# Optimization experiments

Hardware: AMD Instinct MI355X
Metric: run time of the kernel (lower is better)

Reference implementation:

```python
import jax, jax.numpy as jnp
import numpy as np

D_MODEL = 1024
N_HEADS = 16
N_KV = 4
HEAD_DIM = D_MODEL // N_HEADS
B, T, CACHE_LEN = 2, 1024, 1024
MAX_SEQ = 4096
ROPE_BASE = 10000.0


def _rope_tables(max_seq_len=MAX_SEQ, head_dim=HEAD_DIM, base=ROPE_BASE):
    inv_freq = 1.0 / (base ** (np.arange(0, head_dim, 2, dtype=np.float32) / head_dim))
    t = np.arange(max_seq_len, dtype=np.float32)
    freqs = np.outer(t, inv_freq)                      # [S, hd/2]
    emb = np.concatenate([freqs, freqs], axis=-1)      # [S, hd]
    return jnp.asarray(np.cos(emb)), jnp.asarray(np.sin(emb))


def _rotate_half(x):
    x1, x2 = jnp.split(x, 2, axis=-1)
    return jnp.concatenate([-x2, x1], axis=-1)


def setup_inputs() -> dict:
    key = jax.random.key(0)
    ks = jax.random.split(key, 8)
    return {
        "x": jax.random.normal(ks[0], (B, T, D_MODEL), dtype=jnp.float32),
        "k_cache": jax.random.normal(ks[1], (B, N_KV, CACHE_LEN, HEAD_DIM), dtype=jnp.float32),
        "v_cache": jax.random.normal(ks[2], (B, N_KV, CACHE_LEN, HEAD_DIM), dtype=jnp.float32),
        "position_indices": jax.random.randint(ks[3], (B, T), 0, 1024, dtype=jnp.int32),
        "Wq": jax.random.normal(ks[4], (D_MODEL, D_MODEL), dtype=jnp.float32) * 0.02,
        "Wk": jax.random.normal(ks[5], (D_MODEL, N_KV * HEAD_DIM), dtype=jnp.float32) * 0.02,
        "Wv": jax.random.normal(ks[6], (D_MODEL, N_KV * HEAD_DIM), dtype=jnp.float32) * 0.02,
        "Wo": jax.random.normal(ks[7], (D_MODEL, D_MODEL), dtype=jnp.float32) * 0.02,
    }


def reference(x, k_cache, v_cache, position_indices, Wq, Wk, Wv, Wo):
    Bq, Tq, C = x.shape
    n_kv, cache_len, hd = k_cache.shape[1], k_cache.shape[2], k_cache.shape[3]
    n_heads = Wq.shape[1] // hd
    n_rep = n_heads // n_kv
    scale = hd ** -0.5

    cos, sin = _rope_tables()

    # projections -> [B, H, T, hd]
    q = (x @ Wq).reshape(Bq, Tq, n_heads, hd).transpose(0, 2, 1, 3)
    k = (x @ Wk).reshape(Bq, Tq, n_kv, hd).transpose(0, 2, 1, 3)
    v = (x @ Wv).reshape(Bq, Tq, n_kv, hd).transpose(0, 2, 1, 3)

    # progress-aware RoPE: position-indexed gather into tables, offset by cache len
    offset = cache_len
    t_seq = jnp.arange(Tq, dtype=jnp.int32)[None, :] + offset          # [1, T]
    idx = jnp.clip(position_indices.astype(jnp.int32) + t_seq, 0, cos.shape[0] - 1)  # [B, T]
    cos_b = cos[idx][:, None]  # [B, 1, T, hd]
    sin_b = sin[idx][:, None]
    q = q * cos_b + _rotate_half(q) * sin_b
    k = k * cos_b + _rotate_half(k) * sin_b

    # KV-cache concat
    k = jnp.concatenate([k_cache, k], axis=2)  # [B, n_kv, S, hd]
    v = jnp.concatenate([v_cache, v], axis=2)

    # GQA head expansion (repeat each kv head n_rep times, contiguous grouping)
    k_exp = jnp.repeat(k, n_rep, axis=1)  # [B, H, S, hd]
    v_exp = jnp.repeat(v, n_rep, axis=1)

    # manual attention path (k_cache provided -> NO causal mask, matching torch code)
    attn = jnp.einsum("bhtd,bhsd->bhts", q, k_exp) * scale
    attn = jax.nn.softmax(attn, axis=-1)
    out = jnp.einsum("bhts,bhsd->bhtd", attn, v_exp)
    out = out.transpose(0, 2, 1, 3).reshape(Bq, Tq, C)
    return out @ Wo, k, v
```

## Files before the change

kernel.cpp:

```cpp
#include <hip/hip_runtime.h>
#include <hip/hip_bf16.h>
#include <stdint.h>

#define D_MODEL 1024
#define N_HEADS 16
#define N_KV 4
#define HD 64
#define BB 2
#define TT 1024
#define CACHE_LEN 1024
#define SS 2048
#define MAX_SEQ 4096
#define QKV_N 1536
#define NROWS 32768
#define GRP_EL (SS * HD)
#define NSP 4

typedef __attribute__((ext_vector_type(8))) short bf16x8;
typedef __attribute__((ext_vector_type(4))) float f32x4;

__device__ inline short f2bs(float f) {
    __hip_bfloat16 h = __float2bfloat16(f);
    return *reinterpret_cast<short*>(&h);
}
__device__ inline float bs2f(short s) {
    return __uint_as_float((unsigned)(unsigned short)s << 16);
}

__device__ inline int kfrag_off(int s, int d) {
    return (s >> 4) * 1024 + ((d >= 32) ? 512 : 0) + ((((d & 31) >> 3) * 16 + (s & 15)) * 8) + (d & 7);
}
__device__ inline int vfrag_off(int s, int d) {
    return ((s >> 5) * 4 + (d >> 4)) * 512 + ((((s >> 2) & 3) * 16 + (d & 15)) * 8)
         + (((s >> 4) & 1) * 4) + (s & 3);
}

__device__ void transp_body(const float* __restrict__ src, short* __restrict__ dst,
                            int N, int bx, int by) {
    __shared__ short tile[32][34];
    int tx = threadIdx.x & 31, ty = threadIdx.x >> 5;
    int n0 = bx * 32, k0 = by * 32;
#pragma unroll
    for (int i = 0; i < 4; i++)
        tile[ty + i * 8][tx] = f2bs(src[(size_t)(k0 + ty + i * 8) * N + n0 + tx]);
    __syncthreads();
#pragma unroll
    for (int i = 0; i < 4; i++)
        dst[(size_t)(n0 + ty + i * 8) * 1024 + k0 + tx] = tile[tx][ty + i * 8];
}

__global__ void k_prep(const float* __restrict__ x, short* __restrict__ xb,
                       const float* __restrict__ Wq, const float* __restrict__ Wk,
                       const float* __restrict__ Wv, const float* __restrict__ Wo,
                       short* __restrict__ Wt, short* __restrict__ Wot) {
    int id = blockIdx.x;
    if (id < 2048) {
        int i = (id * 256 + threadIdx.x) * 4;
        float4 v = *reinterpret_cast<const float4*>(x + i);
        short4 o = make_short4(f2bs(v.x), f2bs(v.y), f2bs(v.z), f2bs(v.w));
        *reinterpret_cast<short4*>(xb + i) = o;
        return;
    }
    id -= 2048;
    if (id < 1024) { transp_body(Wq, Wt, 1024, id & 31, id >> 5); return; }
    id -= 1024;
    if (id < 256)  { transp_body(Wk, Wt + (size_t)1024 * 1024, 256, id & 7, id >> 3); return; }
    id -= 256;
    if (id < 256)  { transp_body(Wv, Wt + (size_t)1280 * 1024, 256, id & 7, id >> 3); return; }
    id -= 256;
    transp_body(Wo, Wot, 1024, id & 31, id >> 5);
}

template <bool BF16_OUT>
__global__ __launch_bounds__(256) void k_gemm_bt(
    const short* __restrict__ A, const short* __restrict__ Bt, void* __restrict__ Cv,
    int M, int N, int K) {
    __shared__ short sA[64 * 32];
    __shared__ short sB[128 * 32];
    int m0 = blockIdx.y * 64, n0 = blockIdx.x * 128;
    int g = threadIdx.x;
    int lane = g & 63, wave = g >> 6;
    int wr = wave >> 1, wc = wave & 1;
    int quad = lane >> 4, l15 = lane & 15;

    f32x4 acc[2][4] = {};

    for (int k0 = 0; k0 < K; k0 += 32) {
        __syncthreads();
        {
            int row = g >> 2, col = (g & 3) << 3;
            const short* gpA = A + (size_t)(m0 + row) * K + k0 + col;
            __builtin_amdgcn_global_load_lds(
                (const __attribute__((address_space(1))) void*)gpA,
                (__attribute__((address_space(3))) void*)((char*)sA + wave * 1024), 16, 0, 0);
        }
#pragma unroll
        for (int it = 0; it < 2; it++) {
            int c = it * 256 + g;
            int row = c >> 2, col = (c & 3) << 3;
            const short* gpB = Bt + (size_t)(n0 + row) * K + k0 + col;
            __builtin_amdgcn_global_load_lds(
                (const __attribute__((address_space(1))) void*)gpB,
                (__attribute__((address_space(3))) void*)((char*)sB + (it * 256 + wave * 64) * 16), 16, 0, 0);
        }
        __syncthreads();
        bf16x8 af[2], bfr[4];
#pragma unroll
        for (int i = 0; i < 2; i++)
            af[i] = *reinterpret_cast<const bf16x8*>(sA + (wr * 32 + i * 16 + l15) * 32 + quad * 8);
#pragma unroll
        for (int j = 0; j < 4; j++)
            bfr[j] = *reinterpret_cast<const bf16x8*>(sB + (wc * 64 + j * 16 + l15) * 32 + quad * 8);
#pragma unroll
        for (int i = 0; i < 2; i++)
#pragma unroll
            for (int j = 0; j < 4; j++)
                acc[i][j] = __builtin_amdgcn_mfma_f32_16x16x32_bf16(af[i], bfr[j], acc[i][j], 0, 0, 0);
    }
#pragma unroll
    for (int i = 0; i < 2; i++) {
        int m = m0 + wr * 32 + i * 16 + quad * 4;
#pragma unroll
        for (int j = 0; j < 4; j++) {
            int n = n0 + wc * 64 + j * 16 + l15;
#pragma unroll
            for (int r = 0; r < 4; r++) {
                if constexpr (BF16_OUT)
                    ((short*)Cv)[(size_t)(m + r) * N + n] = f2bs(acc[i][j][r]);
                else
                    ((float*)Cv)[(size_t)(m + r) * N + n] = acc[i][j][r];
            }
        }
    }
}

__global__ void k_rope(const short* __restrict__ qkvb, const int* __restrict__ pos,
                       short* __restrict__ qb, short* __restrict__ kf,
                       float* __restrict__ k_out) {
    int row = blockIdx.x;
    int b = row >> 10, t = row & 1023;
    int g = threadIdx.x;
    __shared__ float scv[32], ssv[32];
    if (g < 32) {
        int idx = pos[row] + t + CACHE_LEN;
        idx = min(max(idx, 0), MAX_SEQ - 1);
        float inv = expf(-(float)g * (9.210340371976184f / 32.0f));
        sincosf((float)idx * inv, &ssv[g], &scv[g]);
    }
    __syncthreads();
    const short* src = qkvb + (size_t)row * QKV_N;
    const float QS = 0.18033688011112042f;

#pragma unroll
    for (int p = g; p < 512; p += 256) {
        int h = p >> 5, i = p & 31;
        float cv = scv[i], sv = ssv[i];
        float x1 = bs2f(src[h * 64 + i]), x2 = bs2f(src[h * 64 + i + 32]);
        size_t qbase = ((size_t)(b * N_HEADS + h) * TT + t) * HD;
        qb[qbase + i]      = f2bs((x1 * cv - x2 * sv) * QS);
        qb[qbase + i + 32] = f2bs((x2 * cv + x1 * sv) * QS);
    }
    if (g < 128) {
        int h = g >> 5, i = g & 31;
        float cv = scv[i], sv = ssv[i];
        float x1 = bs2f(src[1024 + h * 64 + i]), x2 = bs2f(src[1024 + h * 64 + i + 32]);
        float o1 = x1 * cv - x2 * sv;
        float o2 = x2 * cv + x1 * sv;
        int s = CACHE_LEN + t;
        size_t kbase = ((size_t)(b * N_KV + h) * SS + s) * HD;
        k_out[kbase + i] = o1;
        k_out[kbase + i + 32] = o2;
        short* kfb = kf + (size_t)(b * N_KV + h) * GRP_EL;
        kfb[kfrag_off(s, i)]      = f2bs(o1);
        kfb[kfrag_off(s, i + 32)] = f2bs(o2);
    }
}

__global__ void k_kv_assemble(const float* __restrict__ k_cache, const float* __restrict__ v_cache,
                              const short* __restrict__ qkvb,
                              float* __restrict__ k_out, float* __restrict__ v_out,
                              short* __restrict__ kf, short* __restrict__ vf) {
    int i = blockIdx.x * 256 + threadIdx.x;
    int d = i & 63;
    int s = (i >> 6) & 2047;
    int bh = i >> 17;
    int b = bh >> 2, h = bh & 3;
    if (s < CACHE_LEN) {
        size_t cidx = ((size_t)bh * CACHE_LEN + s) * HD + d;
        size_t oidx = ((size_t)bh * SS + s) * HD + d;
        float kv = k_cache[cidx];
        float vv = v_cache[cidx];
        k_out[oidx] = kv;
        v_out[oidx] = vv;
        kf[(size_t)bh * GRP_EL + kfrag_off(s, d)] = f2bs(kv);
        vf[(size_t)bh * GRP_EL + vfrag_off(s, d)] = f2bs(vv);
    } else {
        short vb = qkvb[(size_t)(b * TT + (s - CACHE_LEN)) * QKV_N + 1280 + h * 64 + d];
        v_out[((size_t)bh * SS + s) * HD + d] = bs2f(vb);
        vf[(size_t)bh * GRP_EL + vfrag_off(s, d)] = vb;
    }
}

__global__ __launch_bounds__(256) void k_attn(
    const short* __restrict__ qb, const short* __restrict__ kf, const short* __restrict__ vf,
    ushort* __restrict__ po, float* __restrict__ pl) {
    __shared__ short tile[8192];
    int bx = blockIdx.x;
    int sp = bx >> 5;
    int bh = bx & 31;
    int b = bh >> 4, h = bh & 15;
    int hkv = h >> 2;
    int lane = threadIdx.x & 63, wave = threadIdx.x >> 6;
    int quad = lane >> 4, l15 = lane & 15;
    int tw = blockIdx.y * 64 + wave * 16;

    const short* qrow = qb + ((size_t)bh * TT + tw + l15) * HD;
    bf16x8 aq0 = *reinterpret_cast<const bf16x8*>(qrow + quad * 8);
    bf16x8 aq1 = *reinterpret_cast<const bf16x8*>(qrow + 32 + quad * 8);

    const short* kfb = kf + (size_t)(b * N_KV + hkv) * GRP_EL;
    const short* vfb = vf + (size_t)(b * N_KV + hkv) * GRP_EL;

    f32x4 o[4] = {};
    float lr = 0.f;

    int sbeg = sp * (SS / NSP);
    for (int s0 = sbeg; s0 < sbeg + SS / NSP; s0 += 64) {
        __syncthreads();
#pragma unroll
        for (int i = 0; i < 4; i++) {
            int ch = wave * 4 + i;
            const short* src = (ch < 8)
                ? kfb + (s0 >> 4) * 1024 + ch * 512 + lane * 8
                : vfb + (s0 >> 5) * 2048 + (ch - 8) * 512 + lane * 8;
            __builtin_amdgcn_global_load_lds(
                (const __attribute__((address_space(1))) void*)src,
                (__attribute__((address_space(3))) void*)((char*)tile + ch * 1024), 16, 0, 0);
        }
        __syncthreads();

        f32x4 sc[4];
#pragma unroll
        for (int nt = 0; nt < 4; nt++) {
            bf16x8 ak0 = *reinterpret_cast<const bf16x8*>(tile + nt * 1024 + lane * 8);
            bf16x8 ak1 = *reinterpret_cast<const bf16x8*>(tile + nt * 1024 + 512 + lane * 8);
            f32x4 z = {};
            z = __builtin_amdgcn_mfma_f32_16x16x32_bf16(ak0, aq0, z, 0, 0, 0);
            z = __builtin_amdgcn_mfma_f32_16x16x32_bf16(ak1, aq1, z, 0, 0, 0);
            sc[nt] = z;
        }
#pragma unroll
        for (int pp = 0; pp < 2; pp++) {
            bf16x8 bp;
#pragma unroll
            for (int ti = 0; ti < 2; ti++) {
                int nt = pp * 2 + ti;
#pragma unroll
                for (int r = 0; r < 4; r++) {
                    float pv = exp2f(sc[nt][r]);
                    lr += pv;
                    bp[ti * 4 + r] = f2bs(pv);
                }
            }
#pragma unroll
            for (int dt = 0; dt < 4; dt++) {
                bf16x8 av = *reinterpret_cast<const bf16x8*>(
                    tile + 4096 + (pp * 4 + dt) * 512 + lane * 8);
                o[dt] = __builtin_amdgcn_mfma_f32_16x16x32_bf16(av, bp, o[dt], 0, 0, 0);
            }
        }
    }

    lr += __shfl_xor(lr, 16);
    lr += __shfl_xor(lr, 32);

    size_t row = (size_t)bh * TT + tw + l15;
    if (quad == 0) pl[(size_t)sp * NROWS + row] = lr;
#pragma unroll
    for (int dt = 0; dt < 4; dt++) {
        ushort4 w;
        w.x = (ushort)f2bs(o[dt][0]);
        w.y = (ushort)f2bs(o[dt][1]);
        w.z = (ushort)f2bs(o[dt][2]);
        w.w = (ushort)f2bs(o[dt][3]);
        *reinterpret_cast<ushort4*>(po + ((size_t)sp * NROWS + row) * 64 + dt * 16 + quad * 4) = w;
    }
}

__global__ void k_merge(const ushort* __restrict__ po, const float* __restrict__ pl,
                        short* __restrict__ ob) {
    int g = threadIdx.x;
    int row = blockIdx.x * 16 + (g >> 4);
    int d0 = (g & 15) * 4;
    float l = 0.f;
#pragma unroll
    for (int sp = 0; sp < NSP; sp++) l += pl[(size_t)sp * NROWS + row];
    float a0 = 0, a1 = 0, a2 = 0, a3 = 0;
#pragma unroll
    for (int sp = 0; sp < NSP; sp++) {
        ushort4 u = *reinterpret_cast<const ushort4*>(po + ((size_t)sp * NROWS + row) * 64 + d0);
        a0 += __uint_as_float((unsigned)u.x << 16);
        a1 += __uint_as_float((unsigned)u.y << 16);
        a2 += __uint_as_float((unsigned)u.z << 16);
        a3 += __uint_as_float((unsigned)u.w << 16);
    }
    float inv = 1.0f / l;
    int bh = row >> 10, t = row & 1023;
    int b = bh >> 4, h = bh & 15;
    short4 w = make_short4(f2bs(a0 * inv), f2bs(a1 * inv), f2bs(a2 * inv), f2bs(a3 * inv));
    *reinterpret_cast<short4*>(ob + (size_t)(b * TT + t) * D_MODEL + h * 64 + d0) = w;
}

extern "C" void kernel_launch(void* const* d_in, const int* in_sizes, int n_in,
                              void* d_out, int out_size, void* d_ws, size_t ws_size,
                              hipStream_t stream) {
    (void)in_sizes; (void)n_in; (void)out_size; (void)ws_size;
    const float* x       = (const float*)d_in[0];
    const float* k_cache = (const float*)d_in[1];
    const float* v_cache = (const float*)d_in[2];
    const int*   pos     = (const int*)d_in[3];
    const float* Wq      = (const float*)d_in[4];
    const float* Wk      = (const float*)d_in[5];
    const float* Wv      = (const float*)d_in[6];
    const float* Wo      = (const float*)d_in[7];

    float* out   = (float*)d_out;
    float* k_out = out + (size_t)BB * TT * D_MODEL;
    float* v_out = k_out + (size_t)BB * N_KV * SS * HD;

    char* ws = (char*)d_ws;
    short* qkvb = (short*)(ws);
    short* xb   = (short*)(ws + (6u << 20));
    short* Wt   = (short*)(ws + (10u << 20));
    short* qbuf = (short*)(ws + (15u << 20));
    short* kfr  = (short*)(ws + (19u << 20));
    short* vfr  = (short*)(ws + (21u << 20));
    short* obuf = (short*)(ws + (23u << 20));
    short* Wot  = (short*)(ws + (27u << 20));
    float* pl   = (float*)(ws + (29u << 20));
    ushort* po  = (ushort*)(ws);

    k_prep<<<4608, 256, 0, stream>>>(x, xb, Wq, Wk, Wv, Wo, Wt, Wot);

    k_gemm_bt<true><<<dim3(QKV_N / 128, 2048 / 64), 256, 0, stream>>>(
        xb, Wt, qkvb, 2048, QKV_N, 1024);

    k_rope<<<2048, 256, 0, stream>>>(qkvb, pos, qbuf, kfr, k_out);
    k_kv_assemble<<<4096, 256, 0, stream>>>(k_cache, v_cache, qkvb, k_out, v_out, kfr, vfr);

    k_attn<<<dim3(32 * NSP, 16), 256, 0, stream>>>(qbuf, kfr, vfr, po, pl);
    k_merge<<<2048, 256, 0, stream>>>(po, pl, obuf);

    k_gemm_bt<false><<<dim3(1024 / 128, 2048 / 64), 256, 0, stream>>>(
        obuf, Wot, (float*)d_out, 2048, 1024, 1024);
}
```

Baseline: 169.8 us.

## Fuse rope and KV assembly kernels; process two query tiles per attention wave

```diff
diff --git a/kernel.cpp b/kernel.cpp
--- a/kernel.cpp
+++ b/kernel.cpp
@@ -134,53 +134,51 @@
     }
 }
 
-__global__ void k_rope(const short* __restrict__ qkvb, const int* __restrict__ pos,
-                       short* __restrict__ qb, short* __restrict__ kf,
-                       float* __restrict__ k_out) {
-    int row = blockIdx.x;
-    int b = row >> 10, t = row & 1023;
-    int g = threadIdx.x;
-    __shared__ float scv[32], ssv[32];
-    if (g < 32) {
-        int idx = pos[row] + t + CACHE_LEN;
-        idx = min(max(idx, 0), MAX_SEQ - 1);
-        float inv = expf(-(float)g * (9.210340371976184f / 32.0f));
-        sincosf((float)idx * inv, &ssv[g], &scv[g]);
-    }
-    __syncthreads();
-    const short* src = qkvb + (size_t)row * QKV_N;
-    const float QS = 0.18033688011112042f;
-
-#pragma unroll
-    for (int p = g; p < 512; p += 256) {
-        int h = p >> 5, i = p & 31;
-        float cv = scv[i], sv = ssv[i];
-        float x1 = bs2f(src[h * 64 + i]), x2 = bs2f(src[h * 64 + i + 32]);
-        size_t qbase = ((size_t)(b * N_HEADS + h) * TT + t) * HD;
-        qb[qbase + i]      = f2bs((x1 * cv - x2 * sv) * QS);
-        qb[qbase + i + 32] = f2bs((x2 * cv + x1 * sv) * QS);
-    }
-    if (g < 128) {
-        int h = g >> 5, i = g & 31;
-        float cv = scv[i], sv = ssv[i];
-        float x1 = bs2f(src[1024 + h * 64 + i]), x2 = bs2f(src[1024 + h * 64 + i + 32]);
-        float o1 = x1 * cv - x2 * sv;
-        float o2 = x2 * cv + x1 * sv;
-        int s = CACHE_LEN + t;
-        size_t kbase = ((size_t)(b * N_KV + h) * SS + s) * HD;
-        k_out[kbase + i] = o1;
-        k_out[kbase + i + 32] = o2;
-        short* kfb = kf + (size_t)(b * N_KV + h) * GRP_EL;
-        kfb[kfrag_off(s, i)]      = f2bs(o1);
-        kfb[kfrag_off(s, i + 32)] = f2bs(o2);
-    }
-}
-
-__global__ void k_kv_assemble(const float* __restrict__ k_cache, const float* __restrict__ v_cache,
-                              const short* __restrict__ qkvb,
-                              float* __restrict__ k_out, float* __restrict__ v_out,
-                              short* __restrict__ kf, short* __restrict__ vf) {
-    int i = blockIdx.x * 256 + threadIdx.x;
+__global__ void k_post(const short* __restrict__ qkvb, const int* __restrict__ pos,
+                       const float* __restrict__ k_cache, const float* __restrict__ v_cache,
+                       short* __restrict__ qb, short* __restrict__ kf, short* __restrict__ vf,
+                       float* __restrict__ k_out, float* __restrict__ v_out) {
+    int id = blockIdx.x;
+    if (id < 2048) {
+        int row = id;
+        int b = row >> 10, t = row & 1023;
+        int g = threadIdx.x;
+        __shared__ float scv[32], ssv[32];
+        if (g < 32) {
+            int idx = pos[row] + t + CACHE_LEN;
+            idx = min(max(idx, 0), MAX_SEQ - 1);
+            float inv = expf(-(float)g * (9.210340371976184f / 32.0f));
+            sincosf((float)idx * inv, &ssv[g], &scv[g]);
+        }
+        __syncthreads();
+        const short* src = qkvb + (size_t)row * QKV_N;
+        const float QS = 0.18033688011112042f;
+#pragma unroll
+        for (int p = g; p < 512; p += 256) {
+            int h = p >> 5, i = p & 31;
+            float cv = scv[i], sv = ssv[i];
+            float x1 = bs2f(src[h * 64 + i]), x2 = bs2f(src[h * 64 + i + 32]);
+            size_t qbase = ((size_t)(b * N_HEADS + h) * TT + t) * HD;
+            qb[qbase + i]      = f2bs((x1 * cv - x2 * sv) * QS);
+            qb[qbase + i + 32] = f2bs((x2 * cv + x1 * sv) * QS);
+        }
+        if (g < 128) {
+            int h = g >> 5, i = g & 31;
+            float cv = scv[i], sv = ssv[i];
+            float x1 = bs2f(src[1024 + h * 64 + i]), x2 = bs2f(src[1024 + h * 64 + i + 32]);
+            float o1 = x1 * cv - x2 * sv;
+            float o2 = x2 * cv + x1 * sv;
+            int s = CACHE_LEN + t;
+            size_t kbase = ((size_t)(b * N_KV + h) * SS + s) * HD;
+            k_out[kbase + i] = o1;
+            k_out[kbase + i + 32] = o2;
+            short* kfb = kf + (size_t)(b * N_KV + h) * GRP_EL;
+            kfb[kfrag_off(s, i)]      = f2bs(o1);
+            kfb[kfrag_off(s, i + 32)] = f2bs(o2);
+        }
+        return;
+    }
+    int i = (id - 2048) * 256 + threadIdx.x;
     int d = i & 63;
     int s = (i >> 6) & 2047;
     int bh = i >> 17;
@@ -201,7 +199,7 @@
     }
 }
 
-__global__ __launch_bounds__(256) void k_attn(
+__global__ __launch_bounds__(256, 4) void k_attn(
     const short* __restrict__ qb, const short* __restrict__ kf, const short* __restrict__ vf,
     ushort* __restrict__ po, float* __restrict__ pl) {
     __shared__ short tile[8192];
@@ -212,17 +210,21 @@
     int hkv = h >> 2;
     int lane = threadIdx.x & 63, wave = threadIdx.x >> 6;
     int quad = lane >> 4, l15 = lane & 15;
-    int tw = blockIdx.y * 64 + wave * 16;
-
-    const short* qrow = qb + ((size_t)bh * TT + tw + l15) * HD;
-    bf16x8 aq0 = *reinterpret_cast<const bf16x8*>(qrow + quad * 8);
-    bf16x8 aq1 = *reinterpret_cast<const bf16x8*>(qrow + 32 + quad * 8);
+    int tw0 = blockIdx.y * 128 + wave * 16;
+    int tw1 = tw0 + 64;
+
+    const short* qrow0 = qb + ((size_t)bh * TT + tw0 + l15) * HD;
+    const short* qrow1 = qb + ((size_t)bh * TT + tw1 + l15) * HD;
+    bf16x8 aq00 = *reinterpret_cast<const bf16x8*>(qrow0 + quad * 8);
+    bf16x8 aq01 = *reinterpret_cast<const bf16x8*>(qrow0 + 32 + quad * 8);
+    bf16x8 aq10 = *reinterpret_cast<const bf16x8*>(qrow1 + quad * 8);
+    bf16x8 aq11 = *reinterpret_cast<const bf16x8*>(qrow1 + 32 + quad * 8);
 
     const short* kfb = kf + (size_t)(b * N_KV + hkv) * GRP_EL;
     const short* vfb = vf + (size_t)(b * N_KV + hkv) * GRP_EL;
 
-    f32x4 o[4] = {};
-    float lr = 0.f;
+    f32x4 o0[4] = {}, o1[4] = {};
+    float lr0 = 0.f, lr1 = 0.f;
 
     int sbeg = sp * (SS / NSP);
     for (int s0 = sbeg; s0 < sbeg + SS / NSP; s0 += 64) {
@@ -239,51 +241,65 @@
         }
         __syncthreads();
 
-        f32x4 sc[4];
-#pragma unroll
-        for (int nt = 0; nt < 4; nt++) {
-            bf16x8 ak0 = *reinterpret_cast<const bf16x8*>(tile + nt * 1024 + lane * 8);
-            bf16x8 ak1 = *reinterpret_cast<const bf16x8*>(tile + nt * 1024 + 512 + lane * 8);
-            f32x4 z = {};
-            z = __builtin_amdgcn_mfma_f32_16x16x32_bf16(ak0, aq0, z, 0, 0, 0);
-            z = __builtin_amdgcn_mfma_f32_16x16x32_bf16(ak1, aq1, z, 0, 0, 0);
-            sc[nt] = z;
-        }
 #pragma unroll
         for (int pp = 0; pp < 2; pp++) {
-            bf16x8 bp;
+            f32x4 s0c[2], s1c[2];
 #pragma unroll
             for (int ti = 0; ti < 2; ti++) {
                 int nt = pp * 2 + ti;
+                bf16x8 ak0 = *reinterpret_cast<const bf16x8*>(tile + nt * 1024 + lane * 8);
+                bf16x8 ak1 = *reinterpret_cast<const bf16x8*>(tile + nt * 1024 + 512 + lane * 8);
+                f32x4 z = {};
+                z = __builtin_amdgcn_mfma_f32_16x16x32_bf16(ak0, aq00, z, 0, 0, 0);
+                z = __builtin_amdgcn_mfma_f32_16x16x32_bf16(ak1, aq01, z, 0, 0, 0);
+                s0c[ti] = z;
+                f32x4 w = {};
+                w = __builtin_amdgcn_mfma_f32_16x16x32_bf16(ak0, aq10, w, 0, 0, 0);
+                w = __builtin_amdgcn_mfma_f32_16x16x32_bf16(ak1, aq11, w, 0, 0, 0);
+                s1c[ti] = w;
+            }
+            bf16x8 bp0, bp1;
+#pragma unroll
+            for (int ti = 0; ti < 2; ti++)
 #pragma unroll
                 for (int r = 0; r < 4; r++) {
-                    float pv = exp2f(sc[nt][r]);
-                    lr += pv;
-                    bp[ti * 4 + r] = f2bs(pv);
+                    float p0 = exp2f(s0c[ti][r]);
+                    float p1 = exp2f(s1c[ti][r]);
+                    lr0 += p0;
+                    lr1 += p1;
+                    bp0[ti * 4 + r] = f2bs(p0);
+                    bp1[ti * 4 + r] = f2bs(p1);
                 }
-            }
 #pragma unroll
             for (int dt = 0; dt < 4; dt++) {
                 bf16x8 av = *reinterpret_cast<const bf16x8*>(
                     tile + 4096 + (pp * 4 + dt) * 512 + lane * 8);
-                o[dt] = __builtin_amdgcn_mfma_f32_16x16x32_bf16(av, bp, o[dt], 0, 0, 0);
+                o0[dt] = __builtin_amdgcn_mfma_f32_16x16x32_bf16(av, bp0, o0[dt], 0, 0, 0);
+                o1[dt] = __builtin_amdgcn_mfma_f32_16x16x32_bf16(av, bp1, o1[dt], 0, 0, 0);
             }
         }
     }
 
-    lr += __shfl_xor(lr, 16);
-    lr += __shfl_xor(lr, 32);
-
-    size_t row = (size_t)bh * TT + tw + l15;
-    if (quad == 0) pl[(size_t)sp * NROWS + row] = lr;
+    lr0 += __shfl_xor(lr0, 16);
+    lr0 += __shfl_xor(lr0, 32);
+    lr1 += __shfl_xor(lr1, 16);
+    lr1 += __shfl_xor(lr1, 32);
+
+    size_t row0 = (size_t)bh * TT + tw0 + l15;
+    size_t row1 = (size_t)bh * TT + tw1 + l15;
+    if (quad == 0) {
+        pl[(size_t)sp * NROWS + row0] = lr0;
+        pl[(size_t)sp * NROWS + row1] = lr1;
+    }
 #pragma unroll
     for (int dt = 0; dt < 4; dt++) {
-        ushort4 w;
-        w.x = (ushort)f2bs(o[dt][0]);
-        w.y = (ushort)f2bs(o[dt][1]);
-        w.z = (ushort)f2bs(o[dt][2]);
-        w.w = (ushort)f2bs(o[dt][3]);
-        *reinterpret_cast<ushort4*>(po + ((size_t)sp * NROWS + row) * 64 + dt * 16 + quad * 4) = w;
+        ushort4 w0, w1;
+        w0.x = (ushort)f2bs(o0[dt][0]); w0.y = (ushort)f2bs(o0[dt][1]);
+        w0.z = (ushort)f2bs(o0[dt][2]); w0.w = (ushort)f2bs(o0[dt][3]);
+        w1.x = (ushort)f2bs(o1[dt][0]); w1.y = (ushort)f2bs(o1[dt][1]);
+        w1.z = (ushort)f2bs(o1[dt][2]); w1.w = (ushort)f2bs(o1[dt][3]);
+        *reinterpret_cast<ushort4*>(po + ((size_t)sp * NROWS + row0) * 64 + dt * 16 + quad * 4) = w0;
+        *reinterpret_cast<ushort4*>(po + ((size_t)sp * NROWS + row1) * 64 + dt * 16 + quad * 4) = w1;
     }
 }
 
@@ -345,10 +361,10 @@
     k_gemm_bt<true><<<dim3(QKV_N / 128, 2048 / 64), 256, 0, stream>>>(
         xb, Wt, qkvb, 2048, QKV_N, 1024);
 
-    k_rope<<<2048, 256, 0, stream>>>(qkvb, pos, qbuf, kfr, k_out);
-    k_kv_assemble<<<4096, 256, 0, stream>>>(k_cache, v_cache, qkvb, k_out, v_out, kfr, vfr);
-
-    k_attn<<<dim3(32 * NSP, 16), 256, 0, stream>>>(qbuf, kfr, vfr, po, pl);
+    k_post<<<6144, 256, 0, stream>>>(qkvb, pos, k_cache, v_cache,
+                                     qbuf, kfr, vfr, k_out, v_out);
+
+    k_attn<<<dim3(32 * NSP, TT / 128), 256, 0, stream>>>(qbuf, kfr, vfr, po, pl);
     k_merge<<<2048, 256, 0, stream>>>(po, pl, obuf);
 
     k_gemm_bt<false><<<dim3(1024 / 128, 2048 / 64), 256, 0, stream>>>(
```

Result: faster. 165.4 us (-2.6%).
